# Kernel optimization log

Hardware: AMD Instinct MI355X
Metric: run time of the kernel (lower is better)

The kernel has to match this reference:

```python
import jax, jax.numpy as jnp
import numpy as np

N_ATOMS = 21
SIG = 10.0
C = 0.0
STD = 1.0
Q = np.sqrt(5.0) / SIG  # Matern-5/2 length-scale factor


def setup_inputs() -> dict:
    key = jax.random.key(0)
    k1, k2, k3 = jax.random.split(key, 3)
    # geometries: scale so interatomic distances are O(1) and nonzero
    Rs = jax.random.normal(k1, (128, N_ATOMS, 3), dtype=jnp.float32) * 2.0
    # training descriptors are inverse distances -> positive, O(0.1..1)
    xs_train = jax.random.uniform(k2, (4096, 210), dtype=jnp.float32, minval=0.1, maxval=1.0)
    Jx_alphas = jax.random.normal(k3, (4096, 210), dtype=jnp.float32)
    return {"Rs": Rs, "xs_train": xs_train, "Jx_alphas": Jx_alphas}


def reference(Rs, xs_train, Jx_alphas):
    M, n = Rs.shape[0], Rs.shape[1]
    i, j = np.tril_indices(n, k=-1)  # static index sets

    # pairwise atom displacements and safe distances (diag masked, not inf)
    diffs = Rs[:, :, None, :] - Rs[:, None, :, :]            # [M,n,n,3]
    sq = jnp.sum(diffs * diffs, axis=-1)                      # [M,n,n]
    eye = jnp.eye(n, dtype=Rs.dtype)
    dists = jnp.sqrt(sq + eye)                                # diag -> 1 (safe)

    # coulomb_matrix descriptor: inverse distances on strict lower triangle
    xs = 1.0 / dists[:, i, j]                                 # [M,D]

    # distances in descriptor space to all (perm-expanded) training points
    x_diffs = Q * xs[:, None, :] - Q * xs_train               # [M,T,D]
    x_dists = jnp.linalg.norm(x_diffs, axis=-1)               # [M,T]

    exp_xs = (5.0 / (3.0 * SIG * SIG)) * jnp.exp(-x_dists)    # kernel weights
    dot = jnp.einsum('mtd,td->mt', x_diffs, Jx_alphas)        # [M,T]
    exp1 = exp_xs * (1.0 + x_dists)

    F1 = jnp.einsum('mt,mtd->md', exp_xs * dot, x_diffs)      # [M,D]
    F2 = exp1 @ Jx_alphas                                     # [M,D]
    Fs_x = (F1 - F2) * STD

    # expand_tril: symmetric full matrix with zero diagonal
    full = jnp.zeros((M, n, n), dtype=Rs.dtype)
    full = full.at[:, i, j].set(Fs_x).at[:, j, i].set(Fs_x)

    # zero out diagonal contribution (original divides by inf there)
    inv_d3 = (1.0 - eye) / (dists ** 3)
    Fs = jnp.einsum('mab,mabc->mbc', full * inv_d3, diffs)    # [M,n,3]

    Es = C + (jnp.sum(exp1 * dot, axis=-1) / Q) * STD         # [M]
    return Es, Fs
```

## Files before the change

### kernel.cpp

```cpp
#include <hip/hip_runtime.h>
#include <hip/hip_bf16.h>

#define MM 128
#define NA 21
#define DD 210
#define DP 224
#define TT 4096
#define NC 64
#define CHT 64
#define XPAD 20

#define QF   0.22360679774997896f
#define Q2F  0.05f
#define K0E  0.016666666666666666f
#define INVQ 4.47213595499958f

#define OFF_TRP  0
#define OFF_JXP  (OFF_TRP + TT*DP)
#define OFF_TRPT (OFF_JXP + TT*DP)
#define OFF_JXPT (OFF_TRPT + DP*TT)
#define OFF_XSP  (OFF_JXPT + DP*TT)
#define OFF_NT   (OFF_XSP + MM*DP)
#define OFF_CT   (OFF_NT + TT)
#define OFF_NM   (OFF_CT + TT)
#define OFF_S1P  (OFF_NM + MM)
#define OFF_EP   (OFF_S1P + NC*MM)
#define OFF_P1   (OFF_EP + NC*MM)
#define OFF_P2   (OFF_P1 + NC*MM*DP)

__global__ __launch_bounds__(256) void k0_prep(
        const float* __restrict__ tr, const float* __restrict__ jx,
        const float* __restrict__ Rs,
        float* __restrict__ trp, float* __restrict__ jxp,
        float* __restrict__ trpT, float* __restrict__ jxpT,
        float* __restrict__ nt, float* __restrict__ ct,
        float* __restrict__ xsp, float* __restrict__ nmg) {
    __shared__ float S1[16][225];
    __shared__ float S2[16][225];
    int b = blockIdx.x, tid = threadIdx.x;

    if (b < 256) {
        int t0 = b * 16;
        for (int i = tid; i < 16 * 224; i += 256) {
            int t = i / 224, d = i - t * 224;
            float v1 = 0.f, v2 = 0.f;
            if (d < DD) { v1 = tr[(t0 + t) * DD + d]; v2 = jx[(t0 + t) * DD + d]; }
            S1[t][d] = v1; S2[t][d] = v2;
            trp[(t0 + t) * DP + d] = v1;
            jxp[(t0 + t) * DP + d] = v2;
        }
        __syncthreads();
        if (tid < 64) {
            int t = tid & 15, seg = tid >> 4;
            float sn = 0.f, sc = 0.f;
            int d0 = seg * 56;
            for (int d = d0; d < d0 + 56; ++d) {
                float v1 = S1[t][d];
                sn = fmaf(v1, v1, sn);
                sc = fmaf(v1, S2[t][d], sc);
            }
            sn += __shfl_xor(sn, 16); sn += __shfl_xor(sn, 32);
            sc += __shfl_xor(sc, 16); sc += __shfl_xor(sc, 32);
            if (seg == 0) { nt[t0 + t] = sn; ct[t0 + t] = sc; }
        }
        for (int i = tid; i < 224 * 16; i += 256) {
            int d = i >> 4, t = i & 15;
            trpT[d * TT + t0 + t] = S1[t][d];
            jxpT[d * TT + t0 + t] = S2[t][d];
        }
    } else {
        int m = b - 256;
        float* Rl  = &S1[0][0];
        float* red = &S2[0][0];
        if (tid < NA * 3) Rl[tid] = Rs[m * NA * 3 + tid];
        __syncthreads();
        float v = 0.f;
        if (tid < DP) {
            float x = 0.f;
            if (tid < DD) {
                int d = tid;
                int a = (int)((1.0f + sqrtf(8.0f * (float)d + 1.0f)) * 0.5f);
                while (a * (a - 1) / 2 > d) --a;
                while ((a + 1) * a / 2 <= d) ++a;
                int bb = d - a * (a - 1) / 2;
                float dx = Rl[a * 3 + 0] - Rl[bb * 3 + 0];
                float dy = Rl[a * 3 + 1] - Rl[bb * 3 + 1];
                float dz = Rl[a * 3 + 2] - Rl[bb * 3 + 2];
                x = 1.0f / sqrtf(dx * dx + dy * dy + dz * dz);
            }
            xsp[m * DP + tid] = x;
            v = x * x;
        }
        #pragma unroll
        for (int off = 32; off >= 1; off >>= 1) v += __shfl_xor(v, off);
        if ((tid & 63) == 0) red[tid >> 6] = v;
        __syncthreads();
        if (tid == 0) nmg[m] = red[0] + red[1] + red[2] + red[3];
    }
}

#define PA_LOAD(bt, bj, KK) do { \
    _Pragma("unroll") \
    for (int u = 0; u < 8; ++u) { \
        bt[u] = tb[(KK + u) * TT]; \
        bj[u] = jb[(KK + u) * TT]; \
    } } while (0)

#define PA_FMA(bt, bj, KK) do { \
    _Pragma("unroll") \
    for (int u = 0; u < 8; ++u) { \
        float4 a = *(const float4*)&xst[(KK + u) * XPAD + my4]; \
        g1[0] = fmaf(a.x, bt[u], g1[0]); \
        g1[1] = fmaf(a.y, bt[u], g1[1]); \
        g1[2] = fmaf(a.z, bt[u], g1[2]); \
        g1[3] = fmaf(a.w, bt[u], g1[3]); \
        g2[0] = fmaf(a.x, bj[u], g2[0]); \
        g2[1] = fmaf(a.y, bj[u], g2[1]); \
        g2[2] = fmaf(a.z, bj[u], g2[2]); \
        g2[3] = fmaf(a.w, bj[u], g2[3]); \
    } } while (0)

#define PB_LOAD(xa1, xa2, T) do { \
    xa1[0] = *(const float4*)&trp[(t0 + (T)) * DP + d0]; \
    xa1[1] = *(const float4*)&trp[(t0 + (T) + 1) * DP + d0]; \
    xa2[0] = *(const float4*)&jxp[(t0 + (T)) * DP + d0]; \
    xa2[1] = *(const float4*)&jxp[(t0 + (T) + 1) * DP + d0]; } while (0)

#define PB_FMA(xa1, xa2, T) do { \
    _Pragma("unroll") \
    for (int i = 0; i < 4; ++i) { \
        float2 w1p = *(const float2*)&Wl1[my4 + i][(T)]; \
        float2 w2p = *(const float2*)&Wl2[my4 + i][(T)]; \
        a1[i].x = fmaf(w1p.x, xa1[0].x, fmaf(w1p.y, xa1[1].x, a1[i].x)); \
        a1[i].y = fmaf(w1p.x, xa1[0].y, fmaf(w1p.y, xa1[1].y, a1[i].y)); \
        a1[i].z = fmaf(w1p.x, xa1[0].z, fmaf(w1p.y, xa1[1].z, a1[i].z)); \
        a1[i].w = fmaf(w1p.x, xa1[0].w, fmaf(w1p.y, xa1[1].w, a1[i].w)); \
        a2[i].x = fmaf(w2p.x, xa2[0].x, fmaf(w2p.y, xa2[1].x, a2[i].x)); \
        a2[i].y = fmaf(w2p.x, xa2[0].y, fmaf(w2p.y, xa2[1].y, a2[i].y)); \
        a2[i].z = fmaf(w2p.x, xa2[0].z, fmaf(w2p.y, xa2[1].z, a2[i].z)); \
        a2[i].w = fmaf(w2p.x, xa2[0].w, fmaf(w2p.y, xa2[1].w, a2[i].w)); \
    } } while (0)

__global__ __launch_bounds__(256) void k23_fused(
        const float* __restrict__ trp, const float* __restrict__ jxp,
        const float* __restrict__ trpT, const float* __restrict__ jxpT,
        const float* __restrict__ xsp, const float* __restrict__ nt,
        const float* __restrict__ ct, const float* __restrict__ nm,
        float* __restrict__ S1P, float* __restrict__ EP,
        float* __restrict__ P1, float* __restrict__ P2) {
    __shared__ __align__(16) float xst[224 * XPAD];
    __shared__ __align__(16) float Wl1[16][CHT];
    __shared__ __align__(16) float Wl2[16][CHT];
    int tid = threadIdx.x;
    int c = blockIdx.x, m0 = blockIdx.y * 16;
    int t0 = c * CHT;
    int tx = tid & 63, wq = tid >> 6, my4 = wq * 4;
    int mq = m0 + my4;

    for (int i = tid; i < 16 * 224; i += 256) {
        int m = i / 224, k = i - m * 224;
        xst[k * XPAD + m] = xsp[(m0 + m) * DP + k];
    }
    __syncthreads();

    float g1[4] = {0.f, 0.f, 0.f, 0.f};
    float g2[4] = {0.f, 0.f, 0.f, 0.f};
    const float* tb = trpT + t0 + tx;
    const float* jb = jxpT + t0 + tx;
    {
        float p0t[8], p0j[8], p1t[8], p1j[8];
        PA_LOAD(p0t, p0j, 0);
        int k = 0;
        for (; k < DP - 16; k += 16) {
            PA_LOAD(p1t, p1j, k + 8);
            PA_FMA(p0t, p0j, k);
            PA_LOAD(p0t, p0j, k + 16);
            PA_FMA(p1t, p1j, k + 8);
        }
        PA_LOAD(p1t, p1j, DP - 8);
        PA_FMA(p0t, p0j, DP - 16);
        PA_FMA(p1t, p1j, DP - 8);
    }

    float ntv = nt[t0 + tx], ctv = ct[t0 + tx];
    float s1l[4], el[4];
    #pragma unroll
    for (int i = 0; i < 4; ++i) {
        float nmv = nm[mq + i];
        float d2 = Q2F * (nmv + ntv - 2.f * g1[i]);
        float xd = sqrtf(fmaxf(d2, 0.f));
        float e  = K0E * __expf(-xd);
        float dv = QF * (g2[i] - ctv);
        float w1 = e * dv;
        float w2 = e * (1.f + xd);
        Wl1[my4 + i][tx] = w1;
        Wl2[my4 + i][tx] = w2;
        s1l[i] = w1;
        el[i]  = w2 * dv;
    }
    #pragma unroll
    for (int off = 32; off >= 1; off >>= 1) {
        #pragma unroll
        for (int i = 0; i < 4; ++i) {
            s1l[i] += __shfl_xor(s1l[i], off);
            el[i]  += __shfl_xor(el[i], off);
        }
    }
    if (tx == 0) {
        #pragma unroll
        for (int i = 0; i < 4; ++i) {
            S1P[c * MM + mq + i] = s1l[i];
            EP [c * MM + mq + i] = el[i];
        }
    }

    int d0 = 4 * (tx < 56 ? tx : 55);
    bool act = (tx < 56);
    float4 a1[4], a2[4];
    #pragma unroll
    for (int i = 0; i < 4; ++i) { a1[i] = {0.f,0.f,0.f,0.f}; a2[i] = {0.f,0.f,0.f,0.f}; }
    {
        float4 xa1[2], xa2[2], xb1[2], xb2[2];
        PB_LOAD(xa1, xa2, 0);
        int g = 0;
        for (; g < 30; g += 2) {
            PB_LOAD(xb1, xb2, (g + 1) * 2);
            PB_FMA(xa1, xa2, g * 2);
            PB_LOAD(xa1, xa2, (g + 2) * 2);
            PB_FMA(xb1, xb2, (g + 1) * 2);
        }
        PB_LOAD(xb1, xb2, 62);
        PB_FMA(xa1, xa2, 60);
        PB_FMA(xb1, xb2, 62);
    }
    if (act) {
        #pragma unroll
        for (int i = 0; i < 4; ++i) {
            *(float4*)&P1[((size_t)c * MM + mq + i) * DP + d0] = a1[i];
            *(float4*)&P2[((size_t)c * MM + mq + i) * DP + d0] = a2[i];
        }
    }
}

__global__ __launch_bounds__(256) void k4_final(
        const float* __restrict__ Rs, const float* __restrict__ xsp,
        const float* __restrict__ P1, const float* __restrict__ P2,
        const float* __restrict__ S1P, const float* __restrict__ EP,
        float* __restrict__ out) {
    int m = blockIdx.x, tid = threadIdx.x;
    __shared__ float fxs[DD];
    __shared__ float Rl[64];
    __shared__ float sE[2];
    if (tid < NA * 3) Rl[tid] = Rs[m * NA * 3 + tid];
    if (tid >= 64 && tid < 128) {
        int cc = tid - 64;
        float s = S1P[cc * MM + m];
        float e = EP [cc * MM + m];
        #pragma unroll
        for (int off = 32; off >= 1; off >>= 1) {
            s += __shfl_xor(s, off);
            e += __shfl_xor(e, off);
        }
        if (cc == 0) { sE[0] = s; sE[1] = e; }
    }
    float pa = 0.f, pb = 0.f;
    if (tid < DD) {
        #pragma unroll 8
        for (int cc = 0; cc < NC; ++cc) {
            pa += P1[((size_t)cc * MM + m) * DP + tid];
            pb += P2[((size_t)cc * MM + m) * DP + tid];
        }
    }
    __syncthreads();
    if (tid < DD)
        fxs[tid] = QF * xsp[m * DP + tid] * sE[0] - QF * pa - pb;
    __syncthreads();
    if (tid < NA * 3) {
        int b = tid / 3, c = tid - b * 3;
        float acc = 0.f;
        #pragma unroll
        for (int a = 0; a < NA; ++a) {
            if (a == b) continue;
            int hi = a > b ? a : b, lo = a > b ? b : a;
            int d = hi * (hi - 1) / 2 + lo;
            float dx = Rl[a * 3 + 0] - Rl[b * 3 + 0];
            float dy = Rl[a * 3 + 1] - Rl[b * 3 + 1];
            float dz = Rl[a * 3 + 2] - Rl[b * 3 + 2];
            float r2 = dx * dx + dy * dy + dz * dz;
            float ir = 1.0f / sqrtf(r2);
            float w = fxs[d] * ir * ir * ir;
            float comp = (c == 0) ? dx : ((c == 1) ? dy : dz);
            acc = fmaf(w, comp, acc);
        }
        out[MM + m * NA * 3 + tid] = acc;
    }
    if (tid == 0) out[m] = sE[1] * INVQ;
}

extern "C" void kernel_launch(void* const* d_in, const int* in_sizes, int n_in,
                              void* d_out, int out_size, void* d_ws, size_t ws_size,
                              hipStream_t stream) {
    const float* Rs = (const float*)d_in[0];
    const float* tr = (const float*)d_in[1];
    const float* jx = (const float*)d_in[2];
    float* out = (float*)d_out;
    float* ws = (float*)d_ws;

    float* trp  = ws + OFF_TRP;
    float* jxp  = ws + OFF_JXP;
    float* trpT = ws + OFF_TRPT;
    float* jxpT = ws + OFF_JXPT;
    float* xsp  = ws + OFF_XSP;
    float* nt   = ws + OFF_NT;
    float* ct   = ws + OFF_CT;
    float* nm   = ws + OFF_NM;
    float* S1P  = ws + OFF_S1P;
    float* EP   = ws + OFF_EP;
    float* P1   = ws + OFF_P1;
    float* P2   = ws + OFF_P2;

    k0_prep<<<384, 256, 0, stream>>>(tr, jx, Rs, trp, jxp, trpT, jxpT, nt, ct, xsp, nm);
    k23_fused<<<dim3(NC, MM / 16), 256, 0, stream>>>(trp, jxp, trpT, jxpT, xsp, nt, ct, nm, S1P, EP, P1, P2);
    k4_final<<<MM, 256, 0, stream>>>(Rs, xsp, P1, P2, S1P, EP, out);
}
```

Before: 58.08 us.

## Deepen load pipelines, widen prep tiles, split final reduction into two kernels

Several changes land together. The prep kernel now handles 32 training rows per block instead of 16, so it launches fewer blocks. Both GEMM-like phases of the fused kernel move from double to triple and quadruple register buffering of global loads, to hide more memory latency. The final kernel is split into a reduction kernel over (m, d-quarter) blocks, which spreads the 64-chunk partial-sum reads across more blocks, and a separate forces kernel. The split adds a kernel launch and a round trip through workspace memory, and the deeper buffers use more registers.

```diff
diff --git a/kernel.cpp b/kernel.cpp
--- a/kernel.cpp
+++ b/kernel.cpp
@@ -27,6 +27,7 @@
 #define OFF_EP   (OFF_S1P + NC*MM)
 #define OFF_P1   (OFF_EP + NC*MM)
 #define OFF_P2   (OFF_P1 + NC*MM*DP)
+#define OFF_FSX  (OFF_P2 + NC*MM*DP)
 
 __global__ __launch_bounds__(256) void k0_prep(
         const float* __restrict__ tr, const float* __restrict__ jx,
@@ -35,13 +36,13 @@
         float* __restrict__ trpT, float* __restrict__ jxpT,
         float* __restrict__ nt, float* __restrict__ ct,
         float* __restrict__ xsp, float* __restrict__ nmg) {
-    __shared__ float S1[16][225];
-    __shared__ float S2[16][225];
+    __shared__ float S1[32][225];
+    __shared__ float S2[32][225];
     int b = blockIdx.x, tid = threadIdx.x;
 
-    if (b < 256) {
-        int t0 = b * 16;
-        for (int i = tid; i < 16 * 224; i += 256) {
+    if (b < 128) {
+        int t0 = b * 32;
+        for (int i = tid; i < 32 * 224; i += 256) {
             int t = i / 224, d = i - t * 224;
             float v1 = 0.f, v2 = 0.f;
             if (d < DD) { v1 = tr[(t0 + t) * DD + d]; v2 = jx[(t0 + t) * DD + d]; }
@@ -51,25 +52,25 @@
         }
         __syncthreads();
         if (tid < 64) {
-            int t = tid & 15, seg = tid >> 4;
+            int t = tid & 31, h = tid >> 5;
             float sn = 0.f, sc = 0.f;
-            int d0 = seg * 56;
-            for (int d = d0; d < d0 + 56; ++d) {
+            int d0 = h * 112;
+            for (int d = d0; d < d0 + 112; ++d) {
                 float v1 = S1[t][d];
                 sn = fmaf(v1, v1, sn);
                 sc = fmaf(v1, S2[t][d], sc);
             }
-            sn += __shfl_xor(sn, 16); sn += __shfl_xor(sn, 32);
-            sc += __shfl_xor(sc, 16); sc += __shfl_xor(sc, 32);
-            if (seg == 0) { nt[t0 + t] = sn; ct[t0 + t] = sc; }
-        }
-        for (int i = tid; i < 224 * 16; i += 256) {
-            int d = i >> 4, t = i & 15;
+            sn += __shfl_xor(sn, 32);
+            sc += __shfl_xor(sc, 32);
+            if (h == 0) { nt[t0 + t] = sn; ct[t0 + t] = sc; }
+        }
+        for (int i = tid; i < 224 * 32; i += 256) {
+            int d = i >> 5, t = i & 31;
             trpT[d * TT + t0 + t] = S1[t][d];
             jxpT[d * TT + t0 + t] = S2[t][d];
         }
     } else {
-        int m = b - 256;
+        int m = b - 128;
         float* Rl  = &S1[0][0];
         float* red = &S2[0][0];
         if (tid < NA * 3) Rl[tid] = Rs[m * NA * 3 + tid];
@@ -120,25 +121,25 @@
         g2[3] = fmaf(a.w, bj[u], g2[3]); \
     } } while (0)
 
-#define PB_LOAD(xa1, xa2, T) do { \
-    xa1[0] = *(const float4*)&trp[(t0 + (T)) * DP + d0]; \
-    xa1[1] = *(const float4*)&trp[(t0 + (T) + 1) * DP + d0]; \
-    xa2[0] = *(const float4*)&jxp[(t0 + (T)) * DP + d0]; \
-    xa2[1] = *(const float4*)&jxp[(t0 + (T) + 1) * DP + d0]; } while (0)
-
-#define PB_FMA(xa1, xa2, T) do { \
+#define PB_LOAD(x1v, x2v, T) do { \
+    x1v[0] = *(const float4*)&trp[(t0 + (T)) * DP + d0]; \
+    x1v[1] = *(const float4*)&trp[(t0 + (T) + 1) * DP + d0]; \
+    x2v[0] = *(const float4*)&jxp[(t0 + (T)) * DP + d0]; \
+    x2v[1] = *(const float4*)&jxp[(t0 + (T) + 1) * DP + d0]; } while (0)
+
+#define PB_FMA(x1v, x2v, T) do { \
     _Pragma("unroll") \
     for (int i = 0; i < 4; ++i) { \
         float2 w1p = *(const float2*)&Wl1[my4 + i][(T)]; \
         float2 w2p = *(const float2*)&Wl2[my4 + i][(T)]; \
-        a1[i].x = fmaf(w1p.x, xa1[0].x, fmaf(w1p.y, xa1[1].x, a1[i].x)); \
-        a1[i].y = fmaf(w1p.x, xa1[0].y, fmaf(w1p.y, xa1[1].y, a1[i].y)); \
-        a1[i].z = fmaf(w1p.x, xa1[0].z, fmaf(w1p.y, xa1[1].z, a1[i].z)); \
-        a1[i].w = fmaf(w1p.x, xa1[0].w, fmaf(w1p.y, xa1[1].w, a1[i].w)); \
-        a2[i].x = fmaf(w2p.x, xa2[0].x, fmaf(w2p.y, xa2[1].x, a2[i].x)); \
-        a2[i].y = fmaf(w2p.x, xa2[0].y, fmaf(w2p.y, xa2[1].y, a2[i].y)); \
-        a2[i].z = fmaf(w2p.x, xa2[0].z, fmaf(w2p.y, xa2[1].z, a2[i].z)); \
-        a2[i].w = fmaf(w2p.x, xa2[0].w, fmaf(w2p.y, xa2[1].w, a2[i].w)); \
+        a1[i].x = fmaf(w1p.x, x1v[0].x, fmaf(w1p.y, x1v[1].x, a1[i].x)); \
+        a1[i].y = fmaf(w1p.x, x1v[0].y, fmaf(w1p.y, x1v[1].y, a1[i].y)); \
+        a1[i].z = fmaf(w1p.x, x1v[0].z, fmaf(w1p.y, x1v[1].z, a1[i].z)); \
+        a1[i].w = fmaf(w1p.x, x1v[0].w, fmaf(w1p.y, x1v[1].w, a1[i].w)); \
+        a2[i].x = fmaf(w2p.x, x2v[0].x, fmaf(w2p.y, x2v[1].x, a2[i].x)); \
+        a2[i].y = fmaf(w2p.x, x2v[0].y, fmaf(w2p.y, x2v[1].y, a2[i].y)); \
+        a2[i].z = fmaf(w2p.x, x2v[0].z, fmaf(w2p.y, x2v[1].z, a2[i].z)); \
+        a2[i].w = fmaf(w2p.x, x2v[0].w, fmaf(w2p.y, x2v[1].w, a2[i].w)); \
     } } while (0)
 
 __global__ __launch_bounds__(256) void k23_fused(
@@ -168,18 +169,17 @@
     const float* tb = trpT + t0 + tx;
     const float* jb = jxpT + t0 + tx;
     {
-        float p0t[8], p0j[8], p1t[8], p1j[8];
-        PA_LOAD(p0t, p0j, 0);
-        int k = 0;
-        for (; k < DP - 16; k += 16) {
-            PA_LOAD(p1t, p1j, k + 8);
-            PA_FMA(p0t, p0j, k);
-            PA_LOAD(p0t, p0j, k + 16);
-            PA_FMA(p1t, p1j, k + 8);
-        }
-        PA_LOAD(p1t, p1j, DP - 8);
-        PA_FMA(p0t, p0j, DP - 16);
-        PA_FMA(p1t, p1j, DP - 8);
+        float At[8], Aj[8], Bt[8], Bj[8], Ct[8], Cj[8];
+        PA_LOAD(At, Aj, 0);
+        PA_LOAD(Bt, Bj, 8);
+        for (int k8 = 0; k8 < 176; k8 += 24) {
+            PA_LOAD(Ct, Cj, k8 + 16); PA_FMA(At, Aj, k8);
+            PA_LOAD(At, Aj, k8 + 24); PA_FMA(Bt, Bj, k8 + 8);
+            PA_LOAD(Bt, Bj, k8 + 32); PA_FMA(Ct, Cj, k8 + 16);
+        }
+        PA_LOAD(Ct, Cj, 208); PA_FMA(At, Aj, 192);
+        PA_LOAD(At, Aj, 216); PA_FMA(Bt, Bj, 200);
+        PA_FMA(Ct, Cj, 208);  PA_FMA(At, Aj, 216);
     }
 
     float ntv = nt[t0 + tx], ctv = ct[t0 + tx];
@@ -220,18 +220,20 @@
     #pragma unroll
     for (int i = 0; i < 4; ++i) { a1[i] = {0.f,0.f,0.f,0.f}; a2[i] = {0.f,0.f,0.f,0.f}; }
     {
-        float4 xa1[2], xa2[2], xb1[2], xb2[2];
-        PB_LOAD(xa1, xa2, 0);
-        int g = 0;
-        for (; g < 30; g += 2) {
-            PB_LOAD(xb1, xb2, (g + 1) * 2);
-            PB_FMA(xa1, xa2, g * 2);
-            PB_LOAD(xa1, xa2, (g + 2) * 2);
-            PB_FMA(xb1, xb2, (g + 1) * 2);
-        }
-        PB_LOAD(xb1, xb2, 62);
-        PB_FMA(xa1, xa2, 60);
-        PB_FMA(xb1, xb2, 62);
+        float4 A1v[2], A2v[2], B1v[2], B2v[2], C1v[2], C2v[2], D1v[2], D2v[2];
+        PB_LOAD(A1v, A2v, 0);
+        PB_LOAD(B1v, B2v, 2);
+        PB_LOAD(C1v, C2v, 4);
+        for (int s = 0; s < 28; s += 4) {
+            PB_LOAD(D1v, D2v, 2*s + 6);  PB_FMA(A1v, A2v, 2*s);
+            PB_LOAD(A1v, A2v, 2*s + 8);  PB_FMA(B1v, B2v, 2*s + 2);
+            PB_LOAD(B1v, B2v, 2*s + 10); PB_FMA(C1v, C2v, 2*s + 4);
+            PB_LOAD(C1v, C2v, 2*s + 12); PB_FMA(D1v, D2v, 2*s + 6);
+        }
+        PB_LOAD(D1v, D2v, 62); PB_FMA(A1v, A2v, 56);
+        PB_FMA(B1v, B2v, 58);
+        PB_FMA(C1v, C2v, 60);
+        PB_FMA(D1v, D2v, 62);
     }
     if (act) {
         #pragma unroll
@@ -242,38 +244,43 @@
     }
 }
 
-__global__ __launch_bounds__(256) void k4_final(
-        const float* __restrict__ Rs, const float* __restrict__ xsp,
+__global__ __launch_bounds__(64) void k4_reduce(
+        const float* __restrict__ xsp,
         const float* __restrict__ P1, const float* __restrict__ P2,
         const float* __restrict__ S1P, const float* __restrict__ EP,
+        float* __restrict__ Fsx, float* __restrict__ out) {
+    int m = blockIdx.x, dq = blockIdx.y, tid = threadIdx.x;
+    float s = S1P[tid * MM + m];
+    float e = EP [tid * MM + m];
+    #pragma unroll
+    for (int off = 32; off >= 1; off >>= 1) {
+        s += __shfl_xor(s, off);
+        e += __shfl_xor(e, off);
+    }
+    if (tid < 56) {
+        int d = dq * 56 + tid;
+        float pa = 0.f, pb = 0.f;
+        #pragma unroll 8
+        for (int cc = 0; cc < NC; ++cc) {
+            pa += P1[((size_t)cc * MM + m) * DP + d];
+            pb += P2[((size_t)cc * MM + m) * DP + d];
+        }
+        Fsx[m * DP + d] = QF * xsp[m * DP + d] * s - QF * pa - pb;
+    }
+    if (dq == 0 && tid == 63) out[m] = e * INVQ;
+}
+
+__global__ __launch_bounds__(64) void k4_forces(
+        const float* __restrict__ Rs, const float* __restrict__ Fsx,
         float* __restrict__ out) {
     int m = blockIdx.x, tid = threadIdx.x;
-    __shared__ float fxs[DD];
+    __shared__ float fxs[DP];
     __shared__ float Rl[64];
-    __shared__ float sE[2];
     if (tid < NA * 3) Rl[tid] = Rs[m * NA * 3 + tid];
-    if (tid >= 64 && tid < 128) {
-        int cc = tid - 64;
-        float s = S1P[cc * MM + m];
-        float e = EP [cc * MM + m];
-        #pragma unroll
-        for (int off = 32; off >= 1; off >>= 1) {
-            s += __shfl_xor(s, off);
-            e += __shfl_xor(e, off);
-        }
-        if (cc == 0) { sE[0] = s; sE[1] = e; }
-    }
-    float pa = 0.f, pb = 0.f;
-    if (tid < DD) {
-        #pragma unroll 8
-        for (int cc = 0; cc < NC; ++cc) {
-            pa += P1[((size_t)cc * MM + m) * DP + tid];
-            pb += P2[((size_t)cc * MM + m) * DP + tid];
-        }
-    }
-    __syncthreads();
-    if (tid < DD)
-        fxs[tid] = QF * xsp[m * DP + tid] * sE[0] - QF * pa - pb;
+    fxs[tid]       = Fsx[m * DP + tid];
+    fxs[tid + 64]  = Fsx[m * DP + tid + 64];
+    fxs[tid + 128] = Fsx[m * DP + tid + 128];
+    if (tid < 32) fxs[tid + 192] = Fsx[m * DP + tid + 192];
     __syncthreads();
     if (tid < NA * 3) {
         int b = tid / 3, c = tid - b * 3;
@@ -294,7 +301,6 @@
         }
         out[MM + m * NA * 3 + tid] = acc;
     }
-    if (tid == 0) out[m] = sE[1] * INVQ;
 }
 
 extern "C" void kernel_launch(void* const* d_in, const int* in_sizes, int n_in,
@@ -318,8 +324,10 @@
     float* EP   = ws + OFF_EP;
     float* P1   = ws + OFF_P1;
     float* P2   = ws + OFF_P2;
-
-    k0_prep<<<384, 256, 0, stream>>>(tr, jx, Rs, trp, jxp, trpT, jxpT, nt, ct, xsp, nm);
+    float* Fsx  = ws + OFF_FSX;
+
+    k0_prep<<<256, 256, 0, stream>>>(tr, jx, Rs, trp, jxp, trpT, jxpT, nt, ct, xsp, nm);
     k23_fused<<<dim3(NC, MM / 16), 256, 0, stream>>>(trp, jxp, trpT, jxpT, xsp, nt, ct, nm, S1P, EP, P1, P2);
-    k4_final<<<MM, 256, 0, stream>>>(Rs, xsp, P1, P2, S1P, EP, out);
-}
+    k4_reduce<<<dim3(MM, 4), 64, 0, stream>>>(xsp, P1, P2, S1P, EP, Fsx, out);
+    k4_forces<<<MM, 64, 0, stream>>>(Rs, Fsx, out);
+}
```

Result: slower. 82.14 us (+41.4%).
